# Kernel optimization log

Hardware: AMD Instinct MI355X
Metric: run time of the kernel (lower is better)

## Reference

```python
import jax, jax.numpy as jnp
import numpy as np

B, S, C = 65536, 49, 19


def setup_inputs() -> dict:
    key = jax.random.key(0)
    k1, k2, k3, k4, k5 = jax.random.split(key, 5)
    return {
        "H_factor": jax.random.normal(k1, (B, S, C), dtype=jnp.float32),
        "H_hybrid": jax.random.normal(k2, (B, S, C), dtype=jnp.float32),
        "W_alpha": jax.random.normal(k3, (C, C), dtype=jnp.float32),
        "W_beta": jax.random.normal(k4, (C, C), dtype=jnp.float32),
        "W_out": jax.random.normal(k5, (S, C), dtype=jnp.float32),
        "bias": jnp.zeros((1,), dtype=jnp.float32),
    }


def reference(H_factor, H_hybrid, W_alpha, W_beta, W_out, bias):
    # alpha/beta: softmax-gated over last (channel) dim, shapes [B, S, C]
    alpha = jax.nn.softmax(jnp.einsum("bsc,cd->bsd", H_factor, W_alpha), axis=-1)
    beta = jax.nn.softmax(jnp.einsum("bsc,cd->bsd", H_hybrid, W_beta), axis=-1)
    H_final = alpha * H_factor + beta * H_hybrid  # [B, S, C]
    # weighted full reduction over (S, C) -> [B], plus broadcast bias [1]
    u = jnp.sum(H_final * W_out, axis=(1, 2)) + bias
    return jax.nn.sigmoid(u)
```

## Files before the change

### kernel.cpp

```cpp
#include <hip/hip_runtime.h>


#define BB    65536
#define S     49
#define C     19
#define NPAIR (BB * S)
#define PPB   64
#define NBLK  (NPAIR / PPB)

__global__ __launch_bounds__(PPB, 8)
void wfl_main(const float* __restrict__ Hf, const float* __restrict__ Hh,
              const float* __restrict__ Wa, const float* __restrict__ Wb,
              const float* __restrict__ Wo, float* __restrict__ ws)
{
    __shared__ __align__(16) float lh[PPB * C];

    const int lane = threadIdx.x;
    const int blk  = blockIdx.x;
    const int p0   = blk * PPB;
    const int p    = p0 + lane;
    const int b    = p / S;
    const int s    = p - b * S;

    const float* __restrict__ wop = Wo + s * C;
    const float* hp = lh + lane * C;
    float4* l4 = (float4*)lh;

    float part = 0.f;

    {
        const float4* g4 = (const float4*)(Hf + (size_t)p0 * C);
#pragma unroll
        for (int k = 0; k < 5; ++k) {
            int i = lane + k * PPB;
            if (i < (PPB * C) / 4) l4[i] = g4[i];
        }
        __syncthreads();

        float l[C];
#pragma unroll
        for (int d = 0; d < C; ++d) l[d] = 0.f;
#pragma unroll
        for (int c = 0; c < C; ++c) {
            const float h = hp[c];
#pragma unroll
            for (int d = 0; d < C; ++d)
                l[d] = fmaf(h, Wa[c * C + d], l[d]);
        }
        float den = 0.f, num = 0.f;
#pragma unroll
        for (int d = 0; d < C; ++d) {
            const float e = __expf(l[d]);
            den += e;
            num = fmaf(e * hp[d], wop[d], num);
        }
        part = fmaf(num, __builtin_amdgcn_rcpf(den), part);
        __syncthreads();
    }

    {
        const float4* g4 = (const float4*)(Hh + (size_t)p0 * C);
#pragma unroll
        for (int k = 0; k < 5; ++k) {
            int i = lane + k * PPB;
            if (i < (PPB * C) / 4) l4[i] = g4[i];
        }
        __syncthreads();

        float l[C];
#pragma unroll
        for (int d = 0; d < C; ++d) l[d] = 0.f;
#pragma unroll
        for (int c = 0; c < C; ++c) {
            const float h = hp[c];
#pragma unroll
            for (int d = 0; d < C; ++d)
                l[d] = fmaf(h, Wb[c * C + d], l[d]);
        }
        float den = 0.f, num = 0.f;
#pragma unroll
        for (int d = 0; d < C; ++d) {
            const float e = __expf(l[d]);
            den += e;
            num = fmaf(e * hp[d], wop[d], num);
        }
        part = fmaf(num, __builtin_amdgcn_rcpf(den), part);
    }

    const int b0 = p0 / S;
#pragma unroll
    for (int k = 0; k < 3; ++k) {
        float v = ((b - b0) == k) ? part : 0.f;
#pragma unroll
        for (int off = 32; off; off >>= 1) v += __shfl_xor(v, off, 64);
        if (lane == 0 && (b0 + k) < BB) unsafeAtomicAdd(&ws[b0 + k], v);
    }
}

__global__ __launch_bounds__(256)
void wfl_fin(const float* __restrict__ ws, const float* __restrict__ bias,
             float* __restrict__ out)
{
    const int i = blockIdx.x * 256 + threadIdx.x;
    const float u = ws[i] + bias[0];
    out[i] = __builtin_amdgcn_rcpf(1.f + __expf(-u));
}

extern "C" void kernel_launch(void* const* d_in, const int* in_sizes, int n_in,
                              void* d_out, int out_size, void* d_ws, size_t ws_size,
                              hipStream_t stream)
{
    const float* Hf   = (const float*)d_in[0];
    const float* Hh   = (const float*)d_in[1];
    const float* Wa   = (const float*)d_in[2];
    const float* Wb   = (const float*)d_in[3];
    const float* Wo   = (const float*)d_in[4];
    const float* bias = (const float*)d_in[5];
    float* out = (float*)d_out;
    float* acc = (float*)d_ws;

    hipMemsetAsync(acc, 0, BB * sizeof(float), stream);
    wfl_main<<<NBLK, PPB, 0, stream>>>(Hf, Hh, Wa, Wb, Wo, acc);
    wfl_fin<<<BB / 256, 256, 0, stream>>>(acc, bias, out);
}
```

Before: 511.2 us.

## Load both H tiles and W_out into LDS up front with a single barrier

```diff
diff --git a/kernel.cpp b/kernel.cpp
--- a/kernel.cpp
+++ b/kernel.cpp
@@ -8,12 +8,14 @@
 #define PPB   64
 #define NBLK  (NPAIR / PPB)
 
-__global__ __launch_bounds__(PPB, 8)
+__global__ __launch_bounds__(PPB, 6)
 void wfl_main(const float* __restrict__ Hf, const float* __restrict__ Hh,
               const float* __restrict__ Wa, const float* __restrict__ Wb,
               const float* __restrict__ Wo, float* __restrict__ ws)
 {
-    __shared__ __align__(16) float lh[PPB * C];
+    __shared__ __align__(16) float lhf[PPB * C];
+    __shared__ __align__(16) float lhh[PPB * C];
+    __shared__ __align__(16) float lwo[936];
 
     const int lane = threadIdx.x;
     const int blk  = blockIdx.x;
@@ -22,67 +24,79 @@
     const int b    = p / S;
     const int s    = p - b * S;
 
-    const float* __restrict__ wop = Wo + s * C;
-    const float* hp = lh + lane * C;
-    float4* l4 = (float4*)lh;
+    {
+        const float4* gf = (const float4*)(Hf + (size_t)p0 * C);
+        const float4* gh = (const float4*)(Hh + (size_t)p0 * C);
+        const float4* gw = (const float4*)Wo;
+        float4* sf = (float4*)lhf;
+        float4* sh = (float4*)lhh;
+        float4* sw = (float4*)lwo;
+#pragma unroll
+        for (int k = 0; k < 5; ++k) {
+            int i = lane + k * PPB;
+            if (i < 304) { sf[i] = gf[i]; sh[i] = gh[i]; }
+        }
+#pragma unroll
+        for (int k = 0; k < 4; ++k) {
+            int i = lane + k * PPB;
+            if (i < 232) sw[i] = gw[i];
+        }
+        if (lane < 3) lwo[928 + lane] = Wo[928 + lane];
+    }
+    __syncthreads();
+
+    float wo[C];
+#pragma unroll
+    for (int c = 0; c < C; ++c) wo[c] = lwo[s * C + c];
 
     float part = 0.f;
 
     {
-        const float4* g4 = (const float4*)(Hf + (size_t)p0 * C);
+        float h[C];
 #pragma unroll
-        for (int k = 0; k < 5; ++k) {
-            int i = lane + k * PPB;
-            if (i < (PPB * C) / 4) l4[i] = g4[i];
-        }
-        __syncthreads();
+        for (int c = 0; c < C; ++c) h[c] = lhf[lane * C + c];
 
         float l[C];
 #pragma unroll
         for (int d = 0; d < C; ++d) l[d] = 0.f;
 #pragma unroll
         for (int c = 0; c < C; ++c) {
-            const float h = hp[c];
+            const float hc = h[c];
 #pragma unroll
             for (int d = 0; d < C; ++d)
-                l[d] = fmaf(h, Wa[c * C + d], l[d]);
+                l[d] = fmaf(hc, Wa[c * C + d], l[d]);
         }
         float den = 0.f, num = 0.f;
 #pragma unroll
         for (int d = 0; d < C; ++d) {
             const float e = __expf(l[d]);
             den += e;
-            num = fmaf(e * hp[d], wop[d], num);
+            num = fmaf(e, h[d] * wo[d], num);
         }
         part = fmaf(num, __builtin_amdgcn_rcpf(den), part);
-        __syncthreads();
     }
 
     {
-        const float4* g4 = (const float4*)(Hh + (size_t)p0 * C);
+        float h[C];
 #pragma unroll
-        for (int k = 0; k < 5; ++k) {
-            int i = lane + k * PPB;
-            if (i < (PPB * C) / 4) l4[i] = g4[i];
-        }
-        __syncthreads();
+        for (int c = 0; c < C; ++c) h[c] = lhh[lane * C + c];
 
         float l[C];
 #pragma unroll
         for (int d = 0; d < C; ++d) l[d] = 0.f;
 #pragma unroll
         for (int c = 0; c < C; ++c) {
-            const float h = hp[c];
+            const float hc = h[c];
 #pragma unroll
             for (int d = 0; d < C; ++d)
-                l[d] = fmaf(h, Wb[c * C + d], l[d]);
+                l[d] = fmaf(hc, Wb[c * C + d], l[d]);
         }
         float den = 0.f, num = 0.f;
 #pragma unroll
         for (int d = 0; d < C; ++d) {
             const float e = __expf(l[d]);
             den += e;
-            num = fmaf(e * hp[d], wop[d], num);
+            num = fmaf(e, h[d] * wo[d], num);
         }
         part = fmaf(num, __builtin_amdgcn_rcpf(den), part);
     }
```

Result: slower. 558.9 us (+9.3%).
